# Performance work log

Hardware: AMD Instinct MI355X
Metric: run time of the kernel (lower is better)

## Reference

```python
import jax, jax.numpy as jnp
import numpy as np

B, S, H = 1, 2048, 1024
NH, HD = 16, 64          # num heads, head dim (H = NH*HD)
NT = 1024                # param token num (qkv_slot_num = proj_slot_num)


def pattention(x, key_tokens, value_tokens):
    """Pattention with gelu_l2_norm: x:[...,H] -> [...,out]."""
    attn = jnp.einsum('bsh,th->bst', x, key_tokens)          # scale_factor = 1
    g = jax.nn.gelu(attn, approximate=False)                 # torch F.gelu exact
    norm = jnp.linalg.norm(g, axis=-1, keepdims=True)
    w = g / norm * jnp.sqrt(jnp.asarray(g.shape[-1], g.dtype))
    return jnp.einsum('bst,td->bsd', w, value_tokens)


def setup_inputs() -> dict:
    key = jax.random.key(0)
    ks = jax.random.split(key, 9)
    names = ['q_key', 'q_val', 'k_key', 'k_val', 'v_key', 'v_val', 'proj_key', 'proj_val']
    inp = {'x': jax.random.normal(ks[0], (B, S, H), jnp.float32)}
    for i, n in enumerate(names):
        inp[n] = jax.random.normal(ks[i + 1], (NT, H), jnp.float32) * 0.02
    return inp


def reference(x, q_key, q_val, k_key, k_val, v_key, v_val, proj_key, proj_val):
    # Q/K/V via Pattention (token-parameter attention)
    q = pattention(x, q_key, q_val).reshape(B, S, NH, HD)
    k = pattention(x, k_key, k_val).reshape(B, S, NH, HD)
    v = pattention(x, v_key, v_val).reshape(B, S, NH, HD)
    # causal softmax attention, scale = 1/sqrt(head_dim) (flash default)
    scale = 1.0 / jnp.sqrt(jnp.asarray(HD, q.dtype))
    scores = jnp.einsum('bqhd,bkhd->bhqk', q, k) * scale
    causal = jnp.tril(jnp.ones((S, S), dtype=bool))
    scores = jnp.where(causal, scores, jnp.asarray(-1e30, scores.dtype))
    probs = jax.nn.softmax(scores, axis=-1)
    ctx = jnp.einsum('bhqk,bkhd->bqhd', probs, v).reshape(B, S, H)
    # output projection via Pattention
    return pattention(ctx, proj_key, proj_val)
```

## Files before the change

### kernel.cpp

```cpp
#include <hip/hip_runtime.h>
#include <cstdint>
#include <cstddef>

#define S_LEN 2048
#define H_DIM 1024
#define NTOK  1024
#define NHEAD 16
#define HDIM  64
#define NSPLIT 4

typedef __bf16 bf16;
typedef __bf16 bf16x8 __attribute__((ext_vector_type(8)));
typedef __bf16 bf16x4 __attribute__((ext_vector_type(4)));
typedef float  f32x4  __attribute__((ext_vector_type(4)));

#define QSCALE_LOG2E 0.18033688011112042f

static __device__ __forceinline__ f32x4 mfma16(bf16x8 a, bf16x8 b, f32x4 c) {
    return __builtin_amdgcn_mfma_f32_16x16x32_bf16(a, b, c, 0, 0, 0);
}

static __device__ __forceinline__ void async16(const void* gp, void* lp) {
    __builtin_amdgcn_global_load_lds(
        (const __attribute__((address_space(1))) void*)gp,
        (__attribute__((address_space(3))) void*)lp, 16, 0, 0);
}

static __device__ __forceinline__ float fexp2(float x) {
    return __builtin_amdgcn_exp2f(x);
}

struct PrepArgs {
    const float* csrc[6];
    bf16* cdst[6];
    const float* tsrc[4];
    bf16* tdst[4];
};
__global__ __launch_bounds__(256) void prep_kernel(PrepArgs a) {
    __shared__ float t[32][33];
    if (blockIdx.y < 6) {
        const float* __restrict__ s = a.csrc[blockIdx.y];
        bf16* __restrict__ d = a.cdst[blockIdx.y];
        size_t i = ((size_t)blockIdx.x * 256 + threadIdx.x) * 4;
        f32x4 v = *(const f32x4*)&s[i];
        bf16x4 o;
        o[0] = (bf16)v[0]; o[1] = (bf16)v[1]; o[2] = (bf16)v[2]; o[3] = (bf16)v[3];
        *(bf16x4*)&d[i] = o;
    } else {
        const int z = blockIdx.y - 6;
        const float* __restrict__ in = a.tsrc[z];
        bf16* __restrict__ out = a.tdst[z];
        const int bx = (blockIdx.x & 31) * 32, by = (blockIdx.x >> 5) * 32;
        const int x = threadIdx.x & 31, y0 = threadIdx.x >> 5;
#pragma unroll
        for (int j = 0; j < 32; j += 8)
            t[y0 + j][x] = in[(size_t)(by + y0 + j) * 1024 + bx + x];
        __syncthreads();
#pragma unroll
        for (int j = 0; j < 32; j += 8)
            out[(size_t)(bx + y0 + j) * 1024 + by + x] = (bf16)t[x][y0 + j];
    }
}

template <int MODE, typename OutT>
struct GemmArgs {
    const bf16* A[3];
    const bf16* B[3];
    OutT* C[3];
    float* S[3];
    bf16* Ct[3];
    float emul[3];
};

template <int MODE, typename OutT>
__global__ __launch_bounds__(256, 3) void gemm_bt(GemmArgs<MODE, OutT> args) {
    constexpr int Kd = 1024, Nd = 1024, BK = 64;
    const bf16* __restrict__ A = args.A[blockIdx.z];
    const bf16* __restrict__ B = args.B[blockIdx.z];
    OutT* __restrict__ C = args.C[blockIdx.z];
    float* __restrict__ S = args.S[blockIdx.z];
    bf16* __restrict__ Ct = args.Ct[blockIdx.z];
    const float emul = args.emul[blockIdx.z];

    __shared__ __align__(16) bf16 As[2][128 * BK];
    __shared__ __align__(16) bf16 Bs[2][64 * BK];

    const int tid = threadIdx.x;
    const int w = tid >> 6, lane = tid & 63, quad = lane >> 4, m16 = lane & 15;
    const int wm = (w >> 1) * 64, wn = (w & 1) * 32;
    const int bm = blockIdx.y * 128, bn = blockIdx.x * 64;

    const int srow = lane >> 3;
    const int sseg = ((lane & 7) ^ srow) * 8;

    auto stage = [&](int buf, int k0) {
        const bf16* Ab = A + (size_t)bm * Kd + k0;
#pragma unroll
        for (int c = 0; c < 4; ++c) {
            int chunk = w * 4 + c;
            async16(Ab + (size_t)(chunk * 8 + srow) * Kd + sseg,
                    &As[buf][chunk * 512]);
        }
        const bf16* Bb = B + (size_t)bn * Kd + k0;
#pragma unroll
        for (int c = 0; c < 2; ++c) {
            int chunk = w * 2 + c;
            async16(Bb + (size_t)(chunk * 8 + srow) * Kd + sseg,
                    &Bs[buf][chunk * 512]);
        }
    };

    f32x4 acc[4][2] = {};
    stage(0, 0);

    for (int k0 = 0; k0 < Kd; k0 += BK) {
        const int buf = (k0 >> 6) & 1;
        asm volatile("s_waitcnt vmcnt(0)" ::: "memory");
        __syncthreads();
        if (k0 + BK < Kd) stage(buf ^ 1, k0 + BK);

        bf16x8 a[2][4], b[2][2];
#pragma unroll
        for (int kc = 0; kc < 2; ++kc) {
#pragma unroll
            for (int i = 0; i < 4; ++i) {
                int row = wm + i * 16 + m16;
                a[kc][i] = *(const bf16x8*)
                    &As[buf][row * 64 + (((kc * 4 + quad) ^ (row & 7)) << 3)];
            }
#pragma unroll
            for (int j = 0; j < 2; ++j) {
                int row = wn + j * 16 + m16;
                b[kc][j] = *(const bf16x8*)
                    &Bs[buf][row * 64 + (((kc * 4 + quad) ^ (row & 7)) << 3)];
            }
        }
#pragma unroll
        for (int kc = 0; kc < 2; ++kc)
#pragma unroll
            for (int i = 0; i < 4; ++i)
#pragma unroll
                for (int j = 0; j < 2; ++j)
                    acc[i][j] = mfma16(a[kc][i], b[kc][j], acc[i][j]);
    }

    if (MODE == 1) {
        float sq[4][4] = {};
#pragma unroll
        for (int i = 0; i < 4; ++i)
#pragma unroll
            for (int j = 0; j < 2; ++j)
#pragma unroll
                for (int r = 0; r < 4; ++r) {
                    int row = bm + wm + i * 16 + quad * 4 + r;
                    int col = bn + wn + j * 16 + m16;
                    float v = acc[i][j][r];
                    v = 0.5f * v * (1.0f + erff(v * 0.70710678118654752f));
                    C[(size_t)row * Nd + col] = (OutT)v;
                    sq[i][r] += v * v;
                }
#pragma unroll
        for (int i = 0; i < 4; ++i)
#pragma unroll
            for (int r = 0; r < 4; ++r) {
                float s2 = sq[i][r];
                s2 += __shfl_xor(s2, 1);
                s2 += __shfl_xor(s2, 2);
                s2 += __shfl_xor(s2, 4);
                s2 += __shfl_xor(s2, 8);
                if (m16 == 0)
                    atomicAdd(&S[bm + wm + i * 16 + quad * 4 + r], s2);
            }
        return;
    }

    float scl[4][4];
#pragma unroll
    for (int i = 0; i < 4; ++i)
#pragma unroll
        for (int r = 0; r < 4; ++r)
            scl[i][r] =
                32.0f * rsqrtf(S[bm + wm + i * 16 + quad * 4 + r]) * emul;

    if (Ct != nullptr) {
#pragma unroll
        for (int i = 0; i < 4; ++i)
#pragma unroll
            for (int j = 0; j < 2; ++j) {
                int k = bm + wm + i * 16 + quad * 4;
                int col = bn + wn + j * 16 + m16;
                bf16x4 o4;
#pragma unroll
                for (int r = 0; r < 4; ++r)
                    o4[r] = (bf16)(acc[i][j][r] * scl[i][r]);
                int kb = k >> 6, c = (k >> 3) & 7, off = k & 7;
                int pos = ((c ^ (col & 7)) << 3) + off;
                *(bf16x4*)&Ct[(size_t)col * 2048 + kb * 64 + pos] = o4;
            }
        return;
    }

#pragma unroll
    for (int i = 0; i < 4; ++i)
#pragma unroll
        for (int j = 0; j < 2; ++j)
#pragma unroll
            for (int r = 0; r < 4; ++r) {
                int row = bm + wm + i * 16 + quad * 4 + r;
                int col = bn + wn + j * 16 + m16;
                C[(size_t)row * Nd + col] = (OutT)(acc[i][j][r] * scl[i][r]);
            }
}

template <int MODE, typename OutT>
__global__ __launch_bounds__(512) void gemm_bt512(GemmArgs<MODE, OutT> args) {
    constexpr int Kd = 1024, Nd = 1024, BK = 64;
    const bf16* __restrict__ A = args.A[blockIdx.z];
    const bf16* __restrict__ B = args.B[blockIdx.z];
    OutT* __restrict__ C = args.C[blockIdx.z];
    float* __restrict__ S = args.S[blockIdx.z];
    const float emul = args.emul[blockIdx.z];

    __shared__ __align__(16) bf16 As[2][128 * BK];
    __shared__ __align__(16) bf16 Bs[2][64 * BK];

    const int tid = threadIdx.x;
    const int w = tid >> 6, lane = tid & 63, quad = lane >> 4, m16 = lane & 15;
    const int wm = (w >> 1) * 32, wn = (w & 1) * 32;
    const int bm = blockIdx.y * 128, bn = blockIdx.x * 64;

    const int srow = lane >> 3;
    const int sseg = ((lane & 7) ^ srow) * 8;

    auto stage = [&](int buf, int k0) {
        const bf16* Ab = A + (size_t)bm * Kd + k0;
#pragma unroll
        for (int c = 0; c < 2; ++c) {
            int chunk = w * 2 + c;
            async16(Ab + (size_t)(chunk * 8 + srow) * Kd + sseg,
                    &As[buf][chunk * 512]);
        }
        const bf16* Bb = B + (size_t)bn * Kd + k0;
        {
            int chunk = w;
            async16(Bb + (size_t)(chunk * 8 + srow) * Kd + sseg,
                    &Bs[buf][chunk * 512]);
        }
    };

    f32x4 acc[2][2] = {};
    stage(0, 0);

    for (int k0 = 0; k0 < Kd; k0 += BK) {
        const int buf = (k0 >> 6) & 1;
        asm volatile("s_waitcnt vmcnt(0)" ::: "memory");
        __syncthreads();
        if (k0 + BK < Kd) stage(buf ^ 1, k0 + BK);

        bf16x8 a[2][2], b[2][2];
#pragma unroll
        for (int kc = 0; kc < 2; ++kc) {
#pragma unroll
            for (int i = 0; i < 2; ++i) {
                int row = wm + i * 16 + m16;
                a[kc][i] = *(const bf16x8*)
                    &As[buf][row * 64 + (((kc * 4 + quad) ^ (row & 7)) << 3)];
            }
#pragma unroll
            for (int j = 0; j < 2; ++j) {
                int row = wn + j * 16 + m16;
                b[kc][j] = *(const bf16x8*)
                    &Bs[buf][row * 64 + (((kc * 4 + quad) ^ (row & 7)) << 3)];
            }
        }
#pragma unroll
        for (int kc = 0; kc < 2; ++kc)
#pragma unroll
            for (int i = 0; i < 2; ++i)
#pragma unroll
                for (int j = 0; j < 2; ++j)
                    acc[i][j] = mfma16(a[kc][i], b[kc][j], acc[i][j]);
    }

    if (MODE == 1) {
        float sq[2][4] = {};
#pragma unroll
        for (int i = 0; i < 2; ++i)
#pragma unroll
            for (int j = 0; j < 2; ++j)
#pragma unroll
                for (int r = 0; r < 4; ++r) {
                    int row = bm + wm + i * 16 + quad * 4 + r;
                    int col = bn + wn + j * 16 + m16;
                    float v = acc[i][j][r];
                    v = 0.5f * v * (1.0f + erff(v * 0.70710678118654752f));
                    C[(size_t)row * Nd + col] = (OutT)v;
                    sq[i][r] += v * v;
                }
#pragma unroll
        for (int i = 0; i < 2; ++i)
#pragma unroll
            for (int r = 0; r < 4; ++r) {
                float s2 = sq[i][r];
                s2 += __shfl_xor(s2, 1);
                s2 += __shfl_xor(s2, 2);
                s2 += __shfl_xor(s2, 4);
                s2 += __shfl_xor(s2, 8);
                if (m16 == 0)
                    atomicAdd(&S[bm + wm + i * 16 + quad * 4 + r], s2);
            }
        return;
    }

    float scl[2][4];
#pragma unroll
    for (int i = 0; i < 2; ++i)
#pragma unroll
        for (int r = 0; r < 4; ++r)
            scl[i][r] =
                32.0f * rsqrtf(S[bm + wm + i * 16 + quad * 4 + r]) * emul;

#pragma unroll
    for (int i = 0; i < 2; ++i)
#pragma unroll
        for (int j = 0; j < 2; ++j)
#pragma unroll
            for (int r = 0; r < 4; ++r) {
                int row = bm + wm + i * 16 + quad * 4 + r;
                int col = bn + wn + j * 16 + m16;
                C[(size_t)row * Nd + col] = (OutT)(acc[i][j][r] * scl[i][r]);
            }
}

struct FlashArgs {
    const bf16* Q;
    const bf16* K;
    const bf16* VtG;
    bf16* op[NSPLIT];
    float* ml;
};

__global__ __launch_bounds__(256, 4) void flash_kernel(FlashArgs fa) {
    const int bid = blockIdx.x;
    const int idx = bid >> 3;
    const int h = (bid & 7) * 2 + (idx & 1);
    const int pr = (idx >> 1) & 15;
    const int s = idx >> 5;
    const int tid = threadIdx.x;
    const int w = tid >> 6, lane = tid & 63, quad = lane >> 4, m16 = lane & 15;
    const int hOff = h * HDIM;

    __shared__ __align__(16) bf16 Vs[64 * 64];
    __shared__ __align__(16) bf16 Pw[4][16][72];

    const int vrow = tid >> 3, vchunk = (tid & 7) * 8;
    const bf16* VtH = fa.VtG + (size_t)hOff * 2048;
    bf16* __restrict__ Opart = fa.op[s];

#pragma unroll
    for (int ti = 0; ti < 2; ++ti) {
        const int qt = ti ? 31 - pr : pr;
        const int qRow = qt * 64 + w * 16 + m16;
        bf16x8 bq[2];
        bq[0] = *(const bf16x8*)&fa.Q[(size_t)qRow * H_DIM + hOff + quad * 8];
        bq[1] = *(const bf16x8*)&fa.Q[(size_t)qRow * H_DIM + hOff + 32 + quad * 8];

        f32x4 oacc[4] = {};
        float m_i = -1e30f, l_i = 0.0f;

        for (int kt = s; kt <= qt; kt += NSPLIT) {
            const int k0 = kt * 64;
            const bool diag = (kt == qt);
            __syncthreads();
#pragma unroll
            for (int p = 0; p < 2; ++p) {
                int d = vrow + p * 32;
                async16(VtH + (size_t)d * 2048 + k0 + vchunk,
                        &Vs[d * 64 + vchunk]);
            }
            f32x4 sacc[4] = {};
            __builtin_amdgcn_s_setprio(1);
#pragma unroll
            for (int ks = 0; ks < 2; ++ks)
#pragma unroll
                for (int j = 0; j < 4; ++j) {
                    bf16x8 ak = *(const bf16x8*)
                        &fa.K[(size_t)(k0 + j * 16 + m16) * H_DIM + hOff +
                              ks * 32 + quad * 8];
                    sacc[j] = mfma16(ak, bq[ks], sacc[j]);
                }
            __builtin_amdgcn_s_setprio(0);
            float sv[4][4];
            float mx = -1e30f;
#pragma unroll
            for (int j = 0; j < 4; ++j)
#pragma unroll
                for (int rr = 0; rr < 4; ++rr) {
                    float sc = sacc[j][rr];
                    int kcol = k0 + j * 16 + quad * 4 + rr;
                    if (diag && kcol > qRow) sc = -1e30f;
                    sv[j][rr] = sc;
                    mx = fmaxf(mx, sc);
                }
            mx = fmaxf(mx, __shfl_xor(mx, 16));
            mx = fmaxf(mx, __shfl_xor(mx, 32));
            if (!__all(mx - m_i <= 11.5f)) {
                float mnew = fmaxf(m_i, mx);
                float alpha = fexp2(m_i - mnew);
                l_i *= alpha;
#pragma unroll
                for (int jd = 0; jd < 4; ++jd)
#pragma unroll
                    for (int rr = 0; rr < 4; ++rr) oacc[jd][rr] *= alpha;
                m_i = mnew;
            }
            float ls = 0.0f;
#pragma unroll
            for (int j = 0; j < 4; ++j) {
                bf16x4 pk;
#pragma unroll
                for (int rr = 0; rr < 4; ++rr) {
                    float p = fexp2(sv[j][rr] - m_i);
                    ls += p;
                    pk[rr] = (bf16)p;
                }
                *(bf16x4*)&Pw[w][m16][j * 16 + quad * 4] = pk;
            }
            ls += __shfl_xor(ls, 16);
            ls += __shfl_xor(ls, 32);
            l_i += ls;
            asm volatile("s_waitcnt vmcnt(0)" ::: "memory");
            __syncthreads();
            __builtin_amdgcn_s_setprio(1);
#pragma unroll
            for (int ks = 0; ks < 2; ++ks) {
                bf16x8 bp = *(const bf16x8*)&Pw[w][m16][ks * 32 + quad * 8];
#pragma unroll
                for (int jd = 0; jd < 4; ++jd) {
                    int d = jd * 16 + m16;
                    bf16x8 av = *(const bf16x8*)
                        &Vs[d * 64 + (((ks * 4 + quad) ^ (d & 7)) << 3)];
                    oacc[jd] = mfma16(av, bp, oacc[jd]);
                }
            }
            __builtin_amdgcn_s_setprio(0);
        }
#pragma unroll
        for (int jd = 0; jd < 4; ++jd) {
            bf16x4 o4;
#pragma unroll
            for (int rr = 0; rr < 4; ++rr) o4[rr] = (bf16)oacc[jd][rr];
            *(bf16x4*)&Opart[(size_t)qRow * 1024 + hOff + jd * 16 + quad * 4] = o4;
        }
        if (quad == 0) {
            float* p = fa.ml + ((size_t)(s * 2048 + qRow) * 16 + h) * 2;
            p[0] = m_i;
            p[1] = l_i;
        }
    }
}

struct CombArgs {
    const bf16* op[NSPLIT];
    const float* ml;
    bf16* ctx;
};
__global__ __launch_bounds__(256) void combine_kernel(CombArgs ca) {
    const int unit = blockIdx.x * 4 + (threadIdx.x >> 6);
    const int row = unit >> 4, h = unit & 15;
    const int d = threadIdx.x & 63;
    float mv[NSPLIT], lv[NSPLIT], M = -1e30f;
#pragma unroll
    for (int s2 = 0; s2 < NSPLIT; ++s2) {
        const float* p = ca.ml + ((size_t)(s2 * 2048 + row) * 16 + h) * 2;
        mv[s2] = p[0];
        lv[s2] = p[1];
        M = fmaxf(M, mv[s2]);
    }
    float num = 0.0f, den = 0.0f;
#pragma unroll
    for (int s2 = 0; s2 < NSPLIT; ++s2) {
        float e = fexp2(mv[s2] - M);
        den += lv[s2] * e;
        num += e * (float)ca.op[s2][(size_t)row * 1024 + h * 64 + d];
    }
    ca.ctx[(size_t)row * 1024 + h * 64 + d] = (bf16)(num / den);
}

extern "C" void kernel_launch(void* const* d_in, const int* in_sizes, int n_in,
                              void* d_out, int out_size, void* d_ws,
                              size_t ws_size, hipStream_t stream) {
    const float* x = (const float*)d_in[0];
    const float* keysF[4] = {(const float*)d_in[1], (const float*)d_in[3],
                             (const float*)d_in[5], (const float*)d_in[7]};
    const float* valsF[4] = {(const float*)d_in[2], (const float*)d_in[4],
                             (const float*)d_in[6], (const float*)d_in[8]};
    float* out = (float*)d_out;

    char* ws = (char*)d_ws;
    bf16* xb = (bf16*)(ws);
    bf16* g3[3];
    for (int i = 0; i < 3; ++i) g3[i] = (bf16*)(ws + (4ull << 20) + (size_t)i * (4ull << 20));
    bf16* kb16[4], *vT16[4];
    for (int i = 0; i < 4; ++i) {
        kb16[i] = (bf16*)(ws + (16ull << 20) + (size_t)i * (2ull << 20));
        vT16[i] = (bf16*)(ws + (24ull << 20) + (size_t)i * (2ull << 20));
    }
    bf16* qb    = (bf16*)(ws);
    bf16* kbuf  = (bf16*)(ws + (32ull << 20));
    float* mlbuf = (float*)(ws + (20ull << 20));
    bf16* VtG   = (bf16*)(ws + (36ull << 20));
    bf16* ctx   = (bf16*)(ws + (32ull << 20));
    bf16* projg = (bf16*)(ws + (4ull << 20));

    float* SSq = (float*)d_out;
    float* SSp = (float*)(ws + (36ull << 20));

    bf16* opart[NSPLIT];
    for (int i = 0; i < NSPLIT; ++i)
        opart[i] = (bf16*)(ws + (4ull << 20) + (size_t)i * (4ull << 20));

    hipMemsetAsync(SSq, 0, 3 * 2048 * sizeof(float), stream);

    PrepArgs pa;
    pa.csrc[0] = x;             pa.cdst[0] = xb;
    pa.csrc[1] = x + (1 << 20); pa.cdst[1] = xb + (1 << 20);
    for (int i = 0; i < 4; ++i) { pa.csrc[2 + i] = keysF[i]; pa.cdst[2 + i] = kb16[i]; }
    for (int i = 0; i < 4; ++i) { pa.tsrc[i] = valsF[i]; pa.tdst[i] = vT16[i]; }
    prep_kernel<<<dim3(1024, 10), 256, 0, stream>>>(pa);

    GemmArgs<1, bf16> g1;
    for (int z = 0; z < 3; ++z) {
        g1.A[z] = xb; g1.B[z] = kb16[z]; g1.C[z] = g3[z];
        g1.S[z] = SSq + z * 2048; g1.Ct[z] = nullptr; g1.emul[z] = 1.0f;
    }
    gemm_bt<1, bf16><<<dim3(16, 16, 3), 256, 0, stream>>>(g1);

    GemmArgs<2, bf16> g2;
    bf16* qkv[3] = {qb, kbuf, qb };
    for (int z = 0; z < 3; ++z) {
        g2.A[z] = g3[z]; g2.B[z] = vT16[z]; g2.C[z] = qkv[z];
        g2.S[z] = SSq + z * 2048;
        g2.Ct[z] = (z == 2) ? VtG : nullptr;
        g2.emul[z] = (z == 0) ? QSCALE_LOG2E : 1.0f;
    }
    gemm_bt<2, bf16><<<dim3(16, 16, 3), 256, 0, stream>>>(g2);

    FlashArgs fla;
    fla.Q = qb; fla.K = kbuf; fla.VtG = VtG; fla.ml = mlbuf;
    for (int i = 0; i < NSPLIT; ++i) fla.op[i] = opart[i];
    flash_kernel<<<dim3(1024), 256, 0, stream>>>(fla);

    hipMemsetAsync(SSp, 0, 2048 * sizeof(float), stream);

    CombArgs cba;
    for (int i = 0; i < NSPLIT; ++i) cba.op[i] = opart[i];
    cba.ml = mlbuf; cba.ctx = ctx;
    combine_kernel<<<dim3(8192), 256, 0, stream>>>(cba);

    GemmArgs<1, bf16> p1;
    for (int z = 0; z < 3; ++z) {
        p1.A[z] = ctx; p1.B[z] = kb16[3]; p1.C[z] = projg;
        p1.S[z] = SSp; p1.Ct[z] = nullptr; p1.emul[z] = 1.0f;
    }
    gemm_bt512<1, bf16><<<dim3(16, 16, 1), 512, 0, stream>>>(p1);

    GemmArgs<2, float> p2;
    for (int z = 0; z < 3; ++z) {
        p2.A[z] = projg; p2.B[z] = vT16[3]; p2.C[z] = out;
        p2.S[z] = SSp; p2.Ct[z] = nullptr; p2.emul[z] = 1.0f;
    }
    gemm_bt512<2, float><<<dim3(16, 16, 1), 512, 0, stream>>>(p2);
}
```

Before: 236.3 us.

## Give each flash block one query tile and fold memsets into kernels

The flash kernel now handles a single query tile per block instead of a paired (pr, 31-pr) pair, which doubles the grid to 2048 blocks and raises the occupancy hint to 8 blocks per CU. The mask and max/sum reductions are restructured into tree form. The two hipMemsetAsync calls are removed: the prep kernel zeroes the sum-of-squares buffer and the combine kernel zeroes the projection one, and SSp moves to a new workspace offset. Dropping the causal load-balancing pairing may leave blocks with uneven work, and the 8-block occupancy target may force register pressure.

```diff
diff --git a/kernel.cpp b/kernel.cpp
--- a/kernel.cpp
+++ b/kernel.cpp
@@ -35,10 +35,15 @@
     bf16* cdst[6];
     const float* tsrc[4];
     bf16* tdst[4];
+    float* ssq;
 };
 __global__ __launch_bounds__(256) void prep_kernel(PrepArgs a) {
     __shared__ float t[32][33];
     if (blockIdx.y < 6) {
+        if (blockIdx.y == 0 && blockIdx.x == 0) {
+#pragma unroll
+            for (int i = 0; i < 24; ++i) a.ssq[threadIdx.x + i * 256] = 0.0f;
+        }
         const float* __restrict__ s = a.csrc[blockIdx.y];
         bf16* __restrict__ d = a.cdst[blockIdx.y];
         size_t i = ((size_t)blockIdx.x * 256 + threadIdx.x) * 4;
@@ -340,12 +345,12 @@
     float* ml;
 };
 
-__global__ __launch_bounds__(256, 4) void flash_kernel(FlashArgs fa) {
+__global__ __launch_bounds__(256, 8) void flash_kernel(FlashArgs fa) {
     const int bid = blockIdx.x;
     const int idx = bid >> 3;
     const int h = (bid & 7) * 2 + (idx & 1);
-    const int pr = (idx >> 1) & 15;
-    const int s = idx >> 5;
+    const int qt = (idx >> 1) & 31;
+    const int s = idx >> 6;
     const int tid = threadIdx.x;
     const int w = tid >> 6, lane = tid & 63, quad = lane >> 4, m16 = lane & 15;
     const int hOff = h * HDIM;
@@ -357,106 +362,107 @@
     const bf16* VtH = fa.VtG + (size_t)hOff * 2048;
     bf16* __restrict__ Opart = fa.op[s];
 
-#pragma unroll
-    for (int ti = 0; ti < 2; ++ti) {
-        const int qt = ti ? 31 - pr : pr;
-        const int qRow = qt * 64 + w * 16 + m16;
-        bf16x8 bq[2];
-        bq[0] = *(const bf16x8*)&fa.Q[(size_t)qRow * H_DIM + hOff + quad * 8];
-        bq[1] = *(const bf16x8*)&fa.Q[(size_t)qRow * H_DIM + hOff + 32 + quad * 8];
-
-        f32x4 oacc[4] = {};
-        float m_i = -1e30f, l_i = 0.0f;
-
-        for (int kt = s; kt <= qt; kt += NSPLIT) {
-            const int k0 = kt * 64;
-            const bool diag = (kt == qt);
-            __syncthreads();
-#pragma unroll
-            for (int p = 0; p < 2; ++p) {
-                int d = vrow + p * 32;
-                async16(VtH + (size_t)d * 2048 + k0 + vchunk,
-                        &Vs[d * 64 + vchunk]);
-            }
-            f32x4 sacc[4] = {};
-            __builtin_amdgcn_s_setprio(1);
-#pragma unroll
-            for (int ks = 0; ks < 2; ++ks)
-#pragma unroll
-                for (int j = 0; j < 4; ++j) {
-                    bf16x8 ak = *(const bf16x8*)
-                        &fa.K[(size_t)(k0 + j * 16 + m16) * H_DIM + hOff +
-                              ks * 32 + quad * 8];
-                    sacc[j] = mfma16(ak, bq[ks], sacc[j]);
+    const int qRow = qt * 64 + w * 16 + m16;
+    bf16x8 bq[2];
+    bq[0] = *(const bf16x8*)&fa.Q[(size_t)qRow * H_DIM + hOff + quad * 8];
+    bq[1] = *(const bf16x8*)&fa.Q[(size_t)qRow * H_DIM + hOff + 32 + quad * 8];
+
+    f32x4 oacc[4] = {};
+    float m_i = -1e30f, l_i = 0.0f;
+
+    for (int kt = s; kt <= qt; kt += NSPLIT) {
+        const int k0 = kt * 64;
+        const bool diag = (kt == qt);
+        __syncthreads();
+#pragma unroll
+        for (int p = 0; p < 2; ++p) {
+            int d = vrow + p * 32;
+            async16(VtH + (size_t)d * 2048 + k0 + vchunk,
+                    &Vs[d * 64 + vchunk]);
+        }
+        f32x4 sacc[4] = {};
+        __builtin_amdgcn_s_setprio(1);
+#pragma unroll
+        for (int ks = 0; ks < 2; ++ks)
+#pragma unroll
+            for (int j = 0; j < 4; ++j) {
+                bf16x8 ak = *(const bf16x8*)
+                    &fa.K[(size_t)(k0 + j * 16 + m16) * H_DIM + hOff +
+                          ks * 32 + quad * 8];
+                sacc[j] = mfma16(ak, bq[ks], sacc[j]);
+            }
+        __builtin_amdgcn_s_setprio(0);
+        if (diag) {
+#pragma unroll
+            for (int j = 0; j < 4; ++j)
+#pragma unroll
+                for (int rr = 0; rr < 4; ++rr) {
+                    int kcol = k0 + j * 16 + quad * 4 + rr;
+                    if (kcol > qRow) sacc[j][rr] = -1e30f;
                 }
-            __builtin_amdgcn_s_setprio(0);
-            float sv[4][4];
-            float mx = -1e30f;
-#pragma unroll
-            for (int j = 0; j < 4; ++j)
-#pragma unroll
-                for (int rr = 0; rr < 4; ++rr) {
-                    float sc = sacc[j][rr];
-                    int kcol = k0 + j * 16 + quad * 4 + rr;
-                    if (diag && kcol > qRow) sc = -1e30f;
-                    sv[j][rr] = sc;
-                    mx = fmaxf(mx, sc);
-                }
-            mx = fmaxf(mx, __shfl_xor(mx, 16));
-            mx = fmaxf(mx, __shfl_xor(mx, 32));
-            if (!__all(mx - m_i <= 11.5f)) {
-                float mnew = fmaxf(m_i, mx);
-                float alpha = fexp2(m_i - mnew);
-                l_i *= alpha;
-#pragma unroll
-                for (int jd = 0; jd < 4; ++jd)
-#pragma unroll
-                    for (int rr = 0; rr < 4; ++rr) oacc[jd][rr] *= alpha;
-                m_i = mnew;
-            }
-            float ls = 0.0f;
-#pragma unroll
-            for (int j = 0; j < 4; ++j) {
-                bf16x4 pk;
-#pragma unroll
-                for (int rr = 0; rr < 4; ++rr) {
-                    float p = fexp2(sv[j][rr] - m_i);
-                    ls += p;
-                    pk[rr] = (bf16)p;
-                }
-                *(bf16x4*)&Pw[w][m16][j * 16 + quad * 4] = pk;
-            }
-            ls += __shfl_xor(ls, 16);
-            ls += __shfl_xor(ls, 32);
-            l_i += ls;
-            asm volatile("s_waitcnt vmcnt(0)" ::: "memory");
-            __syncthreads();
-            __builtin_amdgcn_s_setprio(1);
-#pragma unroll
-            for (int ks = 0; ks < 2; ++ks) {
-                bf16x8 bp = *(const bf16x8*)&Pw[w][m16][ks * 32 + quad * 8];
-#pragma unroll
-                for (int jd = 0; jd < 4; ++jd) {
-                    int d = jd * 16 + m16;
-                    bf16x8 av = *(const bf16x8*)
-                        &Vs[d * 64 + (((ks * 4 + quad) ^ (d & 7)) << 3)];
-                    oacc[jd] = mfma16(av, bp, oacc[jd]);
-                }
-            }
-            __builtin_amdgcn_s_setprio(0);
-        }
-#pragma unroll
-        for (int jd = 0; jd < 4; ++jd) {
-            bf16x4 o4;
-#pragma unroll
-            for (int rr = 0; rr < 4; ++rr) o4[rr] = (bf16)oacc[jd][rr];
-            *(bf16x4*)&Opart[(size_t)qRow * 1024 + hOff + jd * 16 + quad * 4] = o4;
-        }
-        if (quad == 0) {
-            float* p = fa.ml + ((size_t)(s * 2048 + qRow) * 16 + h) * 2;
-            p[0] = m_i;
-            p[1] = l_i;
-        }
+        }
+        float tj[4];
+#pragma unroll
+        for (int j = 0; j < 4; ++j)
+            tj[j] = fmaxf(fmaxf(sacc[j][0], sacc[j][1]),
+                          fmaxf(sacc[j][2], sacc[j][3]));
+        float mx = fmaxf(fmaxf(tj[0], tj[1]), fmaxf(tj[2], tj[3]));
+        mx = fmaxf(mx, __shfl_xor(mx, 16));
+        mx = fmaxf(mx, __shfl_xor(mx, 32));
+        if (!__all(mx - m_i <= 11.5f)) {
+            float mnew = fmaxf(m_i, mx);
+            float alpha = fexp2(m_i - mnew);
+            l_i *= alpha;
+#pragma unroll
+            for (int jd = 0; jd < 4; ++jd)
+#pragma unroll
+                for (int rr = 0; rr < 4; ++rr) oacc[jd][rr] *= alpha;
+            m_i = mnew;
+        }
+        float lsj[4];
+#pragma unroll
+        for (int j = 0; j < 4; ++j) {
+            bf16x4 pk;
+            float p0 = fexp2(sacc[j][0] - m_i);
+            float p1 = fexp2(sacc[j][1] - m_i);
+            float p2 = fexp2(sacc[j][2] - m_i);
+            float p3 = fexp2(sacc[j][3] - m_i);
+            pk[0] = (bf16)p0; pk[1] = (bf16)p1;
+            pk[2] = (bf16)p2; pk[3] = (bf16)p3;
+            lsj[j] = (p0 + p1) + (p2 + p3);
+            *(bf16x4*)&Pw[w][m16][j * 16 + quad * 4] = pk;
+        }
+        float ls = (lsj[0] + lsj[1]) + (lsj[2] + lsj[3]);
+        ls += __shfl_xor(ls, 16);
+        ls += __shfl_xor(ls, 32);
+        l_i += ls;
+        asm volatile("s_waitcnt vmcnt(0)" ::: "memory");
+        __syncthreads();
+        __builtin_amdgcn_s_setprio(1);
+#pragma unroll
+        for (int ks = 0; ks < 2; ++ks) {
+            bf16x8 bp = *(const bf16x8*)&Pw[w][m16][ks * 32 + quad * 8];
+#pragma unroll
+            for (int jd = 0; jd < 4; ++jd) {
+                int d = jd * 16 + m16;
+                bf16x8 av = *(const bf16x8*)
+                    &Vs[d * 64 + (((ks * 4 + quad) ^ (d & 7)) << 3)];
+                oacc[jd] = mfma16(av, bp, oacc[jd]);
+            }
+        }
+        __builtin_amdgcn_s_setprio(0);
+    }
+#pragma unroll
+    for (int jd = 0; jd < 4; ++jd) {
+        bf16x4 o4;
+#pragma unroll
+        for (int rr = 0; rr < 4; ++rr) o4[rr] = (bf16)oacc[jd][rr];
+        *(bf16x4*)&Opart[(size_t)qRow * 1024 + hOff + jd * 16 + quad * 4] = o4;
+    }
+    if (quad == 0) {
+        float* p = fa.ml + ((size_t)(s * 2048 + qRow) * 16 + h) * 2;
+        p[0] = m_i;
+        p[1] = l_i;
     }
 }
 
@@ -464,8 +470,10 @@
     const bf16* op[NSPLIT];
     const float* ml;
     bf16* ctx;
+    float* ssp;
 };
 __global__ __launch_bounds__(256) void combine_kernel(CombArgs ca) {
+    if (blockIdx.x < 8) ca.ssp[blockIdx.x * 256 + threadIdx.x] = 0.0f;
     const int unit = blockIdx.x * 4 + (threadIdx.x >> 6);
     const int row = unit >> 4, h = unit & 15;
     const int d = threadIdx.x & 63;
@@ -514,19 +522,18 @@
     bf16* projg = (bf16*)(ws + (4ull << 20));
 
     float* SSq = (float*)d_out;
-    float* SSp = (float*)(ws + (36ull << 20));
+    float* SSp = (float*)(ws + (21ull << 20));
 
     bf16* opart[NSPLIT];
     for (int i = 0; i < NSPLIT; ++i)
         opart[i] = (bf16*)(ws + (4ull << 20) + (size_t)i * (4ull << 20));
-
-    hipMemsetAsync(SSq, 0, 3 * 2048 * sizeof(float), stream);
 
     PrepArgs pa;
     pa.csrc[0] = x;             pa.cdst[0] = xb;
     pa.csrc[1] = x + (1 << 20); pa.cdst[1] = xb + (1 << 20);
     for (int i = 0; i < 4; ++i) { pa.csrc[2 + i] = keysF[i]; pa.cdst[2 + i] = kb16[i]; }
     for (int i = 0; i < 4; ++i) { pa.tsrc[i] = valsF[i]; pa.tdst[i] = vT16[i]; }
+    pa.ssq = SSq;
     prep_kernel<<<dim3(1024, 10), 256, 0, stream>>>(pa);
 
     GemmArgs<1, bf16> g1;
@@ -549,13 +556,11 @@
     FlashArgs fla;
     fla.Q = qb; fla.K = kbuf; fla.VtG = VtG; fla.ml = mlbuf;
     for (int i = 0; i < NSPLIT; ++i) fla.op[i] = opart[i];
-    flash_kernel<<<dim3(1024), 256, 0, stream>>>(fla);
-
-    hipMemsetAsync(SSp, 0, 2048 * sizeof(float), stream);
+    flash_kernel<<<dim3(2048), 256, 0, stream>>>(fla);
 
     CombArgs cba;
     for (int i = 0; i < NSPLIT; ++i) cba.op[i] = opart[i];
-    cba.ml = mlbuf; cba.ctx = ctx;
+    cba.ml = mlbuf; cba.ctx = ctx; cba.ssp = SSp;
     combine_kernel<<<dim3(8192), 256, 0, stream>>>(cba);
 
     GemmArgs<1, bf16> p1;
```

After: 268.3 us. +13.6%, slower.
